# Optimization experiments

Hardware: AMD Instinct MI355X
Metric: run time of the kernel (lower is better)

The kernel has to match this reference:

```python
import math
import jax, jax.numpy as jnp
import numpy as np


def _sinkhorn_attn(q, n):
    """Log-domain Sinkhorn-Knopp, eps=1, max_iter=1, uniform marginals.
    cost C = -q @ q^T, so M = (-C + u + v)/eps = S + u + v with S = q q^T.
    Returns transport plan pi = exp(S + u_i + v_j).  q: [B, n, d]."""
    S = jnp.einsum('bnd,bmd->bnm', q, q)            # [B, n, n]
    log_marg = -math.log(n)                          # log(1/n)
    u = log_marg - jax.nn.logsumexp(S, axis=-1)      # [B, n] row update
    v = log_marg - jax.nn.logsumexp(S + u[..., :, None], axis=-2)  # [B, n] col update
    return jnp.exp(S + u[..., :, None] + v[..., None, :])


def reference(x, row_embed, col_embed):
    # x: [B, d, H, W]; row_embed/col_embed: [len_embedding, d//2]
    B, d, H, W = x.shape
    # learned positional embedding: [H, W, d] -> [d, H, W]
    x_emb = col_embed[:W]                             # [W, F]
    y_emb = row_embed[:H]                             # [H, F]
    F = x_emb.shape[-1]
    pos = jnp.concatenate([
        jnp.broadcast_to(x_emb[None, :, :], (H, W, F)),
        jnp.broadcast_to(y_emb[:, None, :], (H, W, F)),
    ], axis=-1).transpose(2, 0, 1)                    # [d, H, W]
    x = x + pos[None]

    n = H * W
    xf = x.reshape(B, d, n).transpose(0, 2, 1)        # [B, n, d] = q = k = v (v unscaled)
    inv_sqrtV = 1.0 / math.sqrt(math.sqrt(d))         # d**-0.25 applied to q and k each
    attn = _sinkhorn_attn(xf * inv_sqrtV, n)          # [B, n, n]
    out = jnp.einsum('bnm,bmd->bnd', attn, xf)        # [B, n, d]
    return out.transpose(0, 2, 1).reshape(B, d, H, W)


def setup_inputs() -> dict:
    key = jax.random.key(0)
    k1, k2, k3 = jax.random.split(key, 3)
    B, d, H, W = 32, 512, 32, 32
    len_emb, F = 32, d // 2
    return {
        'x': jax.random.normal(k1, (B, d, H, W), dtype=jnp.float32),
        'row_embed': jax.random.uniform(k2, (len_emb, F), dtype=jnp.float32),
        'col_embed': jax.random.uniform(k3, (len_emb, F), dtype=jnp.float32),
    }
```

## Files before the change

kernel.cpp:

```cpp
#include <hip/hip_runtime.h>
#include <hip/hip_fp16.h>
#include <math.h>

typedef _Float16 f16;
typedef _Float16 f16x8 __attribute__((ext_vector_type(8)));
typedef _Float16 f16x4 __attribute__((ext_vector_type(4)));
typedef float f32x4 __attribute__((ext_vector_type(4)));

namespace {
constexpr int kB = 32, kD = 512, kN = 1024, kF = 256;
constexpr float kScale = 0.04419417382415922f;
constexpr float kLogMarg = -6.931471805599453f;
constexpr float kMarg = 1.f / 1024.f;
constexpr float kPScale = 16384.f;
constexpr float kPInv = 1.f / 16384.f;
}

__device__ __forceinline__ void gload16(const void* g, void* l) {
  __builtin_amdgcn_global_load_lds(
      (const __attribute__((address_space(1))) void*)g,
      (__attribute__((address_space(3))) void*)l, 16, 0, 0);
}

__global__ __launch_bounds__(256) void k_prep(
    const float* __restrict__ x, const float* __restrict__ re,
    const float* __restrict__ ce, f16* __restrict__ xf,
    f16* __restrict__ xfT, int b0) {
  __shared__ f16 T[64][68];
  const int lb = blockIdx.z;
  const int i0 = blockIdx.x * 64, c0 = blockIdx.y * 64;
  const int t = threadIdx.x;
  const int il = (t & 15) * 4;
  const int cl = t >> 4;
  const size_t xbase = ((size_t)(b0 + lb) * kD) * kN;
#pragma unroll
  for (int p = 0; p < 4; p++) {
    const int c = c0 + cl + 16 * p;
    const int i = i0 + il;
    const float4 xv = *(const float4*)(x + xbase + (size_t)c * kN + i);
    float4 pv;
    if (c < kF) {
      pv.x = ce[((i + 0) & 31) * kF + c];
      pv.y = ce[((i + 1) & 31) * kF + c];
      pv.z = ce[((i + 2) & 31) * kF + c];
      pv.w = ce[((i + 3) & 31) * kF + c];
    } else {
      const float r = re[(i >> 5) * kF + (c - kF)];
      pv.x = r; pv.y = r; pv.z = r; pv.w = r;
    }
    const f16 h0 = (f16)(xv.x + pv.x), h1 = (f16)(xv.y + pv.y);
    const f16 h2 = (f16)(xv.z + pv.z), h3 = (f16)(xv.w + pv.w);
    f16* dT = xfT + ((size_t)lb * kD + c) * kN + i;
    *(f16x4*)dT = (f16x4){h0, h1, h2, h3};
    T[cl + 16 * p][il + 0] = h0; T[cl + 16 * p][il + 1] = h1;
    T[cl + 16 * p][il + 2] = h2; T[cl + 16 * p][il + 3] = h3;
  }
  __syncthreads();
#pragma unroll
  for (int p = 0; p < 4; p++) {
    const int ir = cl + 16 * p;
    const int cc = il;
    const f16 h0 = T[cc + 0][ir], h1 = T[cc + 1][ir];
    const f16 h2 = T[cc + 2][ir], h3 = T[cc + 3][ir];
    f16* dF = xf + ((size_t)lb * kN + i0 + ir) * kD + c0 + cc;
    *(f16x4*)dF = (f16x4){h0, h1, h2, h3};
  }
}

__global__ __launch_bounds__(256) void k_gemm_s(
    const f16* __restrict__ xf, f16* __restrict__ S16,
    float* __restrict__ rp) {
  __shared__ char sm[65536];
  const int nwg = (int)(gridDim.x * gridDim.z);
  const int lin = (int)(blockIdx.x + gridDim.x * blockIdx.z);
  const int wid = (lin & 7) * (nwg >> 3) + (lin >> 3);
  const int bz = wid / 36;
  int qq = wid - bz * 36;
  int by = 0;
  while (qq >= 8 - by) { qq -= 8 - by; by++; }
  const int bx = by + qq;

  const int lb = bz;
  const int i0 = by * 128, j0 = bx * 128;
  const char* base = (const char*)(xf + (size_t)lb * kN * kD);
  const int t = threadIdx.x;
  const int w = t >> 6, lane = t & 63;
  const int m_off = (w >> 1) * 64, n_off = (w & 1) * 64;
  const int quad = lane >> 4, l15 = lane & 15;
  const int swz = (l15 & 7) << 4;

  int srcA[4], srcB[4], ldsw[4];
#pragma unroll
  for (int p = 0; p < 4; p++) {
    const int off = p * 4096 + w * 1024 + lane * 16;
    const int r = off >> 7;
    const int cb = (off & 127) ^ ((r & 7) << 4);
    srcA[p] = (i0 + r) * (kD * 2) + cb;
    srcB[p] = (j0 + r) * (kD * 2) + cb;
    ldsw[p] = p * 4096 + w * 1024;
  }

  f32x4 acc[4][4];
#pragma unroll
  for (int a = 0; a < 4; a++)
#pragma unroll
    for (int b = 0; b < 4; b++) acc[a][b] = (f32x4){0.f, 0.f, 0.f, 0.f};

#pragma unroll
  for (int p = 0; p < 4; p++) gload16(base + srcA[p], sm + ldsw[p]);
#pragma unroll
  for (int p = 0; p < 4; p++) gload16(base + srcB[p], sm + 16384 + ldsw[p]);
  __syncthreads();

#pragma unroll
  for (int tt = 0; tt < 8; tt++) {
    const int cur = tt & 1, nxt = cur ^ 1;
    if (tt + 1 < 8) {
      const int k0b = (tt + 1) * 128;
#pragma unroll
      for (int p = 0; p < 4; p++)
        gload16(base + srcA[p] + k0b, sm + (nxt << 15) + ldsw[p]);
#pragma unroll
      for (int p = 0; p < 4; p++)
        gload16(base + srcB[p] + k0b, sm + (nxt << 15) + 16384 + ldsw[p]);
    }
    const char* bA = sm + (cur << 15);
    const char* bB = bA + 16384;
#pragma unroll
    for (int kk = 0; kk < 2; kk++) {
      f16x8 af[4], bf[4];
#pragma unroll
      for (int q = 0; q < 4; q++)
        af[q] = *(const f16x8*)(bA + (m_off + 16 * q + l15) * 128 +
                                ((kk * 64 + quad * 16) ^ swz));
#pragma unroll
      for (int q = 0; q < 4; q++)
        bf[q] = *(const f16x8*)(bB + (n_off + 16 * q + l15) * 128 +
                                ((kk * 64 + quad * 16) ^ swz));
#pragma unroll
      for (int qa = 0; qa < 4; qa++)
#pragma unroll
        for (int qb = 0; qb < 4; qb++)
          acc[qa][qb] = __builtin_amdgcn_mfma_f32_16x16x32_f16(
              af[qa], bf[qb], acc[qa][qb], 0, 0, 0);
    }
    __syncthreads();
  }

  f16* Sb = S16 + (size_t)lb * kN * kN;
  const int jt2 = bx * 2 + (w & 1);
  float* rpb = rp + ((size_t)lb * 16 + jt2) * kN + i0 + m_off;
  const bool offd = (bx != by);
  float cs[4] = {0.f, 0.f, 0.f, 0.f};
#pragma unroll
  for (int qa = 0; qa < 4; qa++) {
    const int i = i0 + m_off + 16 * qa + quad * 4;
    float rs[4] = {0.f, 0.f, 0.f, 0.f};
#pragma unroll
    for (int qb = 0; qb < 4; qb++) {
      const int j = j0 + n_off + 16 * qb + l15;
      f16 h4[4];
#pragma unroll
      for (int r = 0; r < 4; r++) {
        const f16 h = (f16)(acc[qa][qb][r] * kScale);
        Sb[(size_t)(i + r) * kN + j] = h;
        h4[r] = h;
        const float e = __expf((float)h);
        rs[r] += e;
        cs[qb] += e;
      }
      if (offd)
        *(f16x4*)(Sb + (size_t)j * kN + i) = (f16x4){h4[0], h4[1], h4[2], h4[3]};
    }
#pragma unroll
    for (int r = 0; r < 4; r++) {
      float s = rs[r];
      s += __shfl_xor(s, 1);
      s += __shfl_xor(s, 2);
      s += __shfl_xor(s, 4);
      s += __shfl_xor(s, 8);
      if (l15 == 0) rpb[16 * qa + 4 * quad + r] = s;
    }
  }
  if (offd) {
    float* rpm = rp + ((size_t)lb * 16 + (by * 2 + (w >> 1))) * kN;
#pragma unroll
    for (int qb = 0; qb < 4; qb++) {
      float s = cs[qb];
      s += __shfl_xor(s, 16);
      s += __shfl_xor(s, 32);
      if (quad == 0) rpm[j0 + n_off + 16 * qb + l15] = s;
    }
  }
}

__global__ __launch_bounds__(256) void k_cs(
    const f16* __restrict__ S16, const float* __restrict__ rp,
    float* __restrict__ u, float* __restrict__ cp) {
  __shared__ float us[64];
  const int lb = blockIdx.z;
  const int seg = blockIdx.y;
  const int tid = threadIdx.x;
  if (tid < 64) {
    const float* r = rp + (size_t)lb * 16 * kN + seg * 64 + tid;
    float s = 0.f;
#pragma unroll
    for (int t = 0; t < 16; t++) s += r[(size_t)t * kN];
    const float uu = kLogMarg - __logf(s);
    us[tid] = uu;
    u[lb * kN + seg * 64 + tid] = uu;
  }
  __syncthreads();
  const int j = tid * 4;
  const f16* Sb = S16 + (size_t)lb * kN * kN + (size_t)(seg * 64) * kN + j;
  float s0 = 0.f, s1 = 0.f, s2 = 0.f, s3 = 0.f;
#pragma unroll 8
  for (int r = 0; r < 64; r++) {
    const f16x4 v = *(const f16x4*)(Sb + (size_t)r * kN);
    const float ur = us[r];
    s0 += __expf((float)v[0] + ur);
    s1 += __expf((float)v[1] + ur);
    s2 += __expf((float)v[2] + ur);
    s3 += __expf((float)v[3] + ur);
  }
  float4 o = {s0, s1, s2, s3};
  *(float4*)(cp + ((size_t)lb * 16 + seg) * kN + j) = o;
}

__global__ __launch_bounds__(256) void k_pt(
    const f16* __restrict__ S16, const float* __restrict__ u,
    const float* __restrict__ cp, f16* __restrict__ t16) {
  __shared__ float us[64];
  const int seg = blockIdx.x;
  const int lb = blockIdx.y;
  const int tid = threadIdx.x;
  const int j = tid * 4;
  const float* c = cp + (size_t)lb * 16 * kN + j;
  float s0 = 0.f, s1 = 0.f, s2 = 0.f, s3 = 0.f;
#pragma unroll
  for (int r = 0; r < 16; r++) {
    const float4 v = *(const float4*)(c + (size_t)r * kN);
    s0 += v.x; s1 += v.y; s2 += v.z; s3 += v.w;
  }
  const float e0 = kMarg / s0, e1 = kMarg / s1;
  const float e2 = kMarg / s2, e3 = kMarg / s3;
  if (tid < 64) us[tid] = u[lb * kN + seg * 64 + tid];
  __syncthreads();
  const f16* Sb = S16 + (size_t)lb * kN * kN + (size_t)(seg * 64) * kN + j;
  f16* Tb = t16 + (size_t)lb * kN * kN + (size_t)(seg * 64) * kN + j;
#pragma unroll 4
  for (int r = 0; r < 64; r++) {
    const f16x4 v = *(const f16x4*)(Sb + (size_t)r * kN);
    const float ur = us[r];
    f16x4 o;
    o[0] = (f16)(__expf((float)v[0] + ur) * e0 * kPScale);
    o[1] = (f16)(__expf((float)v[1] + ur) * e1 * kPScale);
    o[2] = (f16)(__expf((float)v[2] + ur) * e2 * kPScale);
    o[3] = (f16)(__expf((float)v[3] + ur) * e3 * kPScale);
    *(f16x4*)(Tb + (size_t)r * kN) = o;
  }
}

#define AF_READ(q)                                                          \
  _Pragma("unroll")                                                         \
  for (int pa = 0; pa < 2; pa++)                                            \
    _Pragma("unroll")                                                       \
    for (int kk = 0; kk < 2; kk++)                                          \
      af[pa][kk] = *(const f16x8*)(bA + (m_off + 32*(q) + 16*pa + l15)*128  \
                                   + ((kk*64 + quad*16) ^ swz));

#define MFMA_PH(q)                                                          \
  __builtin_amdgcn_s_setprio(1);                                            \
  _Pragma("unroll")                                                         \
  for (int pa = 0; pa < 2; pa++)                                            \
    _Pragma("unroll")                                                       \
    for (int qb = 0; qb < 4; qb++)                                          \
      _Pragma("unroll")                                                     \
      for (int kk = 0; kk < 2; kk++)                                        \
        acc[2*(q)+pa][qb] = __builtin_amdgcn_mfma_f32_16x16x32_f16(         \
            af[pa][kk], bf[qb][kk], acc[2*(q)+pa][qb], 0, 0, 0);            \
  __builtin_amdgcn_s_setprio(0);

__global__ __launch_bounds__(512) void k_gemm_o(
    const f16* __restrict__ xfT, const f16* __restrict__ P,
    float* __restrict__ out, int b0) {
  __shared__ char sm[131072];
  const int nwg = (int)(gridDim.x * gridDim.y * gridDim.z);
  const int lin = (int)(blockIdx.x +
                        gridDim.x * (blockIdx.y + gridDim.y * blockIdx.z));
  const int wid = (lin & 7) * (nwg >> 3) + (lin >> 3);
  const int bx = wid & 3, by = (wid >> 2) & 1, bz = wid >> 3;

  const int lb = bz;
  const int i0 = bx * 256, c0 = by * 256;
  const char* Ab = (const char*)(xfT + (size_t)lb * kD * kN);
  const char* Bb = (const char*)(P + (size_t)lb * kN * kN);
  const int t = threadIdx.x;
  const int w = t >> 6, lane = t & 63;
  const int wm = w >> 2, wn = w & 3;
  const int m_off = wm * 128, n_off = wn * 64;
  const int quad = lane >> 4, l15 = lane & 15;
  const int swz = (l15 & 7) << 4;

  int srcA[4], srcB[4], ldsw[4];
#pragma unroll
  for (int p = 0; p < 4; p++) {
    const int off = p * 8192 + t * 16;
    const int r = off >> 7;
    const int cb = (off & 127) ^ ((r & 7) << 4);
    srcA[p] = (c0 + r) * (kN * 2) + cb;
    srcB[p] = (i0 + r) * (kN * 2) + cb;
    ldsw[p] = p * 8192 + w * 1024;
  }

#pragma unroll
  for (int p = 0; p < 4; p++) gload16(Bb + srcB[p], sm + 65536 + ldsw[p]);
  gload16(Ab + srcA[0], sm + ldsw[0]);
  gload16(Ab + srcA[2], sm + ldsw[2]);
  gload16(Ab + srcA[1], sm + ldsw[1]);
  gload16(Ab + srcA[3], sm + ldsw[3]);
#pragma unroll
  for (int p = 0; p < 4; p++)
    gload16(Bb + srcB[p] + 128, sm + 65536 + 32768 + ldsw[p]);
  f32x4 acc[8][4];
#pragma unroll
  for (int a = 0; a < 8; a++)
#pragma unroll
    for (int b = 0; b < 4; b++) acc[a][b] = (f32x4){0.f, 0.f, 0.f, 0.f};
  asm volatile("s_waitcnt vmcnt(6)" ::: "memory");
  __builtin_amdgcn_s_barrier();
  __builtin_amdgcn_sched_barrier(0);

#pragma unroll
  for (int tt = 0; tt < 16; tt++) {
    const int cur = tt & 1, nxt = cur ^ 1;
    const char* bA = sm + cur * 32768;
    const char* bB = sm + 65536 + cur * 32768;
    char* wA = sm + nxt * 32768;
    char* wB = sm + 65536 + cur * 32768;
    const int kA = (tt + 1) * 128, kBB = (tt + 2) * 128;
    f16x8 bf[4][2], af[2][2];
#pragma unroll
    for (int qb = 0; qb < 4; qb++)
#pragma unroll
      for (int kk = 0; kk < 2; kk++)
        bf[qb][kk] = *(const f16x8*)(bB + (n_off + 16 * qb + l15) * 128 +
                                     ((kk * 64 + quad * 16) ^ swz));
    AF_READ(0)
    asm volatile("s_waitcnt lgkmcnt(0)" ::: "memory");
    __builtin_amdgcn_sched_barrier(0);
    __builtin_amdgcn_s_barrier();
    MFMA_PH(0)
    if (tt + 1 < 16) {
      gload16(Ab + srcA[0] + kA, wA + ldsw[0]);
      gload16(Ab + srcA[2] + kA, wA + ldsw[2]);
    }
    AF_READ(1)
    __builtin_amdgcn_s_barrier();
    MFMA_PH(1)
    if (tt == 15) { asm volatile("s_waitcnt vmcnt(0)" ::: "memory"); }
    else          { asm volatile("s_waitcnt vmcnt(6)" ::: "memory"); }
    __builtin_amdgcn_s_barrier();
    __builtin_amdgcn_sched_barrier(0);
    AF_READ(2)
    __builtin_amdgcn_s_barrier();
    MFMA_PH(2)
    if (tt + 1 < 16) {
      gload16(Ab + srcA[1] + kA, wA + ldsw[1]);
      gload16(Ab + srcA[3] + kA, wA + ldsw[3]);
    }
    if (tt + 2 < 16) {
#pragma unroll
      for (int p = 0; p < 4; p++)
        gload16(Bb + srcB[p] + kBB, wB + ldsw[p]);
    }
    AF_READ(3)
    __builtin_amdgcn_s_barrier();
    MFMA_PH(3)
    if (tt + 2 < 16)      { asm volatile("s_waitcnt vmcnt(6)" ::: "memory"); }
    else if (tt + 1 < 16) { asm volatile("s_waitcnt vmcnt(2)" ::: "memory"); }
    __builtin_amdgcn_s_barrier();
    __builtin_amdgcn_sched_barrier(0);
  }

  float* ob = out + ((size_t)(b0 + lb) * kD) * kN;
#pragma unroll
  for (int qa = 0; qa < 8; qa++) {
    const int c = c0 + m_off + 16 * qa + quad * 4;
#pragma unroll
    for (int qb = 0; qb < 4; qb++) {
      const int i = i0 + n_off + 16 * qb + l15;
#pragma unroll
      for (int r = 0; r < 4; r++)
        ob[(size_t)(c + r) * kN + i] = acc[qa][qb][r] * kPInv;
    }
  }
}

extern "C" void kernel_launch(void* const* d_in, const int* in_sizes, int n_in,
                              void* d_out, int out_size, void* d_ws, size_t ws_size,
                              hipStream_t stream) {
  const float* x = (const float*)d_in[0];
  const float* re = (const float*)d_in[1];
  const float* ce = (const float*)d_in[2];
  float* out = (float*)d_out;

  char* wsb = (char*)d_ws;
  const size_t perb = 2097152ull + 1048576 + 1048576 + 2097152 +
                      4096 + 65536 + 65536;
  int G = (int)(ws_size / perb);
  if (G >= 32) G = 32;
  else if (G >= 16) G = 16;
  else if (G >= 8) G = 8;
  else if (G >= 4) G = 4;
  else if (G < 1) G = 1;
  f16* S16 = (f16*)wsb;
  f16* xf = (f16*)(wsb + (size_t)G * 2097152);
  f16* xfT = (f16*)((char*)xf + (size_t)G * 1048576);
  f16* t16 = (f16*)((char*)xfT + (size_t)G * 1048576);
  float* u = (float*)((char*)t16 + (size_t)G * 2097152);
  float* rp = u + (size_t)G * kN;
  float* cp = rp + (size_t)G * 16 * kN;

  for (int b0 = 0; b0 < kB; b0 += G) {
    const int g = (kB - b0 < G) ? (kB - b0) : G;
    k_prep<<<dim3(16, 8, g), 256, 0, stream>>>(x, re, ce, xf, xfT, b0);
    k_gemm_s<<<dim3(36, 1, g), 256, 0, stream>>>(xf, S16, rp);
    k_cs<<<dim3(1, 16, g), 256, 0, stream>>>(S16, rp, u, cp);
    k_pt<<<dim3(16, g), 256, 0, stream>>>(S16, u, cp, t16);
    k_gemm_o<<<dim3(4, 2, g), 512, 0, stream>>>(xfT, t16, out, b0);
  }
}
```

Baseline: 232.0 us.

## Fuse Sinkhorn column normalization and exp into output GEMM B-tile staging

Removes the separate k_pt kernel that materialized the normalized transport plan in fp16. k_gemm_o now loads raw S16 tiles into LDS and applies exp(S+u)*colscale in place before the MFMA reads, with column scales and row potentials precomputed into shared memory. This eliminates a full write and reread of the n×n plan per batch and one launch. In exchange it adds exp work inside the GEMM loop, duplicates it across the two output column blocks, and adds an extra barrier per k-step.

Result: slower. 243.6 us (+5.0%).

```diff
diff --git a/kernel.cpp b/kernel.cpp
--- a/kernel.cpp
+++ b/kernel.cpp
@@ -227,40 +227,6 @@
   *(float4*)(cp + ((size_t)lb * 16 + seg) * kN + j) = o;
 }
 
-__global__ __launch_bounds__(256) void k_pt(
-    const f16* __restrict__ S16, const float* __restrict__ u,
-    const float* __restrict__ cp, f16* __restrict__ t16) {
-  __shared__ float us[64];
-  const int seg = blockIdx.x;
-  const int lb = blockIdx.y;
-  const int tid = threadIdx.x;
-  const int j = tid * 4;
-  const float* c = cp + (size_t)lb * 16 * kN + j;
-  float s0 = 0.f, s1 = 0.f, s2 = 0.f, s3 = 0.f;
-#pragma unroll
-  for (int r = 0; r < 16; r++) {
-    const float4 v = *(const float4*)(c + (size_t)r * kN);
-    s0 += v.x; s1 += v.y; s2 += v.z; s3 += v.w;
-  }
-  const float e0 = kMarg / s0, e1 = kMarg / s1;
-  const float e2 = kMarg / s2, e3 = kMarg / s3;
-  if (tid < 64) us[tid] = u[lb * kN + seg * 64 + tid];
-  __syncthreads();
-  const f16* Sb = S16 + (size_t)lb * kN * kN + (size_t)(seg * 64) * kN + j;
-  f16* Tb = t16 + (size_t)lb * kN * kN + (size_t)(seg * 64) * kN + j;
-#pragma unroll 4
-  for (int r = 0; r < 64; r++) {
-    const f16x4 v = *(const f16x4*)(Sb + (size_t)r * kN);
-    const float ur = us[r];
-    f16x4 o;
-    o[0] = (f16)(__expf((float)v[0] + ur) * e0 * kPScale);
-    o[1] = (f16)(__expf((float)v[1] + ur) * e1 * kPScale);
-    o[2] = (f16)(__expf((float)v[2] + ur) * e2 * kPScale);
-    o[3] = (f16)(__expf((float)v[3] + ur) * e3 * kPScale);
-    *(f16x4*)(Tb + (size_t)r * kN) = o;
-  }
-}
-
 #define AF_READ(q)                                                          \
   _Pragma("unroll")                                                         \
   for (int pa = 0; pa < 2; pa++)                                            \
@@ -282,9 +248,10 @@
   __builtin_amdgcn_s_setprio(0);
 
 __global__ __launch_bounds__(512) void k_gemm_o(
-    const f16* __restrict__ xfT, const f16* __restrict__ P,
+    const f16* __restrict__ xfT, const f16* __restrict__ S16,
+    const float* __restrict__ u, const float* __restrict__ cp,
     float* __restrict__ out, int b0) {
-  __shared__ char sm[131072];
+  __shared__ char sm[136192];
   const int nwg = (int)(gridDim.x * gridDim.y * gridDim.z);
   const int lin = (int)(blockIdx.x +
                         gridDim.x * (blockIdx.y + gridDim.y * blockIdx.z));
@@ -294,7 +261,7 @@
   const int lb = bz;
   const int i0 = bx * 256, c0 = by * 256;
   const char* Ab = (const char*)(xfT + (size_t)lb * kD * kN);
-  const char* Bb = (const char*)(P + (size_t)lb * kN * kN);
+  const char* Bb = (const char*)(S16 + (size_t)lb * kN * kN);
   const int t = threadIdx.x;
   const int w = t >> 6, lane = t & 63;
   const int wm = w >> 2, wn = w & 3;
@@ -313,6 +280,25 @@
     ldsw[p] = p * 8192 + w * 1024;
   }
 
+  float* evl = (float*)(sm + 131072);
+  float* us = (float*)(sm + 131072 + 4096);
+  {
+    const int j2 = t * 2;
+    const float* c = cp + (size_t)lb * 16 * kN + j2;
+    float s0 = 0.f, s1 = 0.f;
+#pragma unroll
+    for (int r = 0; r < 16; r++) {
+      const float2 v = *(const float2*)(c + (size_t)r * kN);
+      s0 += v.x; s1 += v.y;
+    }
+    evl[j2] = kMarg / s0;
+    evl[j2 + 1] = kMarg / s1;
+    if (t < 256) us[t] = u[lb * kN + i0 + t];
+  }
+  asm volatile("s_waitcnt vmcnt(0) lgkmcnt(0)" ::: "memory");
+  __builtin_amdgcn_sched_barrier(0);
+  __builtin_amdgcn_s_barrier();
+
 #pragma unroll
   for (int p = 0; p < 4; p++) gload16(Bb + srcB[p], sm + 65536 + ldsw[p]);
   gload16(Ab + srcA[0], sm + ldsw[0]);
@@ -327,19 +313,44 @@
   for (int a = 0; a < 8; a++)
 #pragma unroll
     for (int b = 0; b < 4; b++) acc[a][b] = (f32x4){0.f, 0.f, 0.f, 0.f};
-  asm volatile("s_waitcnt vmcnt(6)" ::: "memory");
-  __builtin_amdgcn_s_barrier();
+  asm volatile("s_waitcnt vmcnt(4)" ::: "memory");
   __builtin_amdgcn_sched_barrier(0);
 
 #pragma unroll
   for (int tt = 0; tt < 16; tt++) {
     const int cur = tt & 1, nxt = cur ^ 1;
     const char* bA = sm + cur * 32768;
-    const char* bB = sm + 65536 + cur * 32768;
+    char* bBw = sm + 65536 + cur * 32768;
+    const char* bB = bBw;
     char* wA = sm + nxt * 32768;
     char* wB = sm + 65536 + cur * 32768;
     const int kA = (tt + 1) * 128, kBB = (tt + 2) * 128;
     f16x8 bf[4][2], af[2][2];
+#pragma unroll
+    for (int p = 0; p < 4; p++) {
+      const int off = p * 8192 + t * 16;
+      const int r = off >> 7;
+      const int cbl = (off & 127) ^ ((r & 7) << 4);
+      f16* bp = (f16*)(bBw + off);
+      const f16x8 v = *(const f16x8*)bp;
+      const float ur = us[r];
+      const float* ep = evl + tt * 64 + (cbl >> 1);
+      const float4 e0 = *(const float4*)ep;
+      const float4 e1 = *(const float4*)(ep + 4);
+      f16x8 o;
+      o[0] = (f16)(__expf((float)v[0] + ur) * e0.x * kPScale);
+      o[1] = (f16)(__expf((float)v[1] + ur) * e0.y * kPScale);
+      o[2] = (f16)(__expf((float)v[2] + ur) * e0.z * kPScale);
+      o[3] = (f16)(__expf((float)v[3] + ur) * e0.w * kPScale);
+      o[4] = (f16)(__expf((float)v[4] + ur) * e1.x * kPScale);
+      o[5] = (f16)(__expf((float)v[5] + ur) * e1.y * kPScale);
+      o[6] = (f16)(__expf((float)v[6] + ur) * e1.z * kPScale);
+      o[7] = (f16)(__expf((float)v[7] + ur) * e1.w * kPScale);
+      *(f16x8*)bp = o;
+    }
+    asm volatile("s_waitcnt lgkmcnt(0)" ::: "memory");
+    __builtin_amdgcn_sched_barrier(0);
+    __builtin_amdgcn_s_barrier();
 #pragma unroll
     for (int qb = 0; qb < 4; qb++)
 #pragma unroll
@@ -406,8 +417,7 @@
   float* out = (float*)d_out;
 
   char* wsb = (char*)d_ws;
-  const size_t perb = 2097152ull + 1048576 + 1048576 + 2097152 +
-                      4096 + 65536 + 65536;
+  const size_t perb = 2097152ull + 1048576 + 1048576 + 4096 + 65536 + 65536;
   int G = (int)(ws_size / perb);
   if (G >= 32) G = 32;
   else if (G >= 16) G = 16;
@@ -417,8 +427,7 @@
   f16* S16 = (f16*)wsb;
   f16* xf = (f16*)(wsb + (size_t)G * 2097152);
   f16* xfT = (f16*)((char*)xf + (size_t)G * 1048576);
-  f16* t16 = (f16*)((char*)xfT + (size_t)G * 1048576);
-  float* u = (float*)((char*)t16 + (size_t)G * 2097152);
+  float* u = (float*)((char*)xfT + (size_t)G * 1048576);
   float* rp = u + (size_t)G * kN;
   float* cp = rp + (size_t)G * 16 * kN;
 
@@ -427,7 +436,6 @@
     k_prep<<<dim3(16, 8, g), 256, 0, stream>>>(x, re, ce, xf, xfT, b0);
     k_gemm_s<<<dim3(36, 1, g), 256, 0, stream>>>(xf, S16, rp);
     k_cs<<<dim3(1, 16, g), 256, 0, stream>>>(S16, rp, u, cp);
-    k_pt<<<dim3(16, g), 256, 0, stream>>>(S16, u, cp, t16);
-    k_gemm_o<<<dim3(4, 2, g), 512, 0, stream>>>(xfT, t16, out, b0);
-  }
-}
+    k_gemm_o<<<dim3(4, 2, g), 512, 0, stream>>>(xfT, S16, u, cp, out, b0);
+  }
+}
```
